# Kernel optimization log

Hardware: AMD Instinct MI355X
Metric: run time of the kernel (lower is better)

The kernel has to match this reference:

```python
import jax, jax.numpy as jnp
import numpy as np

ITERS = 5          # iter_node_counts
N, M, Z, E = 68, 46, 384, 368   # base VNs, base CNs, lifting size, total base edges
LLR_CLIP = 20.0    # allowed_llr_range.abs
BIG = 1e9


def setup_inputs() -> dict:
    key = jax.random.key(0)
    k1, k2, k3 = jax.random.split(key, 3)
    B = 64
    # channel LLRs, realistic AWGN-ish magnitudes
    xa = jax.random.normal(k1, (B, N, Z), dtype=jnp.float32) * 4.0
    edge_vn = jax.random.randint(k2, (E,), 0, N, dtype=jnp.int32)
    # regular check degree 8 so every check has >=2 edges (valid min-sum extrinsics)
    edge_cn = (jnp.arange(E, dtype=jnp.int32) % M)
    edge_shift = jax.random.randint(k3, (E,), 0, Z, dtype=jnp.int32)  # circulant shifts
    cn_weight = jnp.ones((ITERS,), dtype=jnp.float32)  # scalar CN weight per iteration
    return {"xa": xa, "cn_weight": cn_weight, "edge_vn": edge_vn,
            "edge_cn": edge_cn, "edge_shift": edge_shift}


def _qms5(x):
    # QMS q_bit=5 quantizer with straight-through estimator
    q = jnp.clip(jnp.round(x * 2.0) / 2.0, -7.5, 7.5)
    xc = jnp.clip(x, -7.5, 7.5)
    return xc + jax.lax.stop_gradient(q - xc)


def _decode(xa, cn_weight, edge_vn, edge_cn, edge_shift):
    B = xa.shape[0]
    xa_in = jnp.transpose(xa, (0, 2, 1))  # [B, Z, N]
    z = jnp.arange(Z)
    # lifting (Lift_Matrix1): cyclic shift each edge's Z copies; unlift is inverse
    idx_lift = ((z[:, None] - edge_shift[None, :]) % Z)[None]    # [1, Z, E]
    idx_unlift = ((z[:, None] + edge_shift[None, :]) % Z)[None]  # [1, Z, E]
    c2v = jnp.zeros((B, Z, E), dtype=xa.dtype)  # prev_llr (CN->VN messages)
    ch = jnp.moveaxis(xa_in, 2, 0)  # [N, B, Z]
    outs = []
    for it in range(ITERS):
        # --- odd layer (VN update): W_skipconn2even + W_odd2even ---
        vn_sum = jax.ops.segment_sum(jnp.moveaxis(c2v, 2, 0), edge_vn, num_segments=N)  # [N,B,Z]
        tot = ch + vn_sum                                  # total belief per VN
        v2c = jnp.moveaxis(tot[edge_vn], 0, 2) - c2v       # extrinsic, [B,Z,E]
        v2c = jnp.clip(v2c, -LLR_CLIP, LLR_CLIP)           # allowed_llr_range
        v2c = jnp.take_along_axis(v2c, idx_lift, axis=1)   # Lift_Matrix1
        # --- even layer (CN update, min-sum): W_even2odd ---
        vE = jnp.moveaxis(v2c, 2, 0)                       # [E, B, Z]
        mag = jnp.abs(vE)
        neg = (vE < 0).astype(jnp.int32)
        cnt = jax.ops.segment_sum(neg, edge_cn, num_segments=M)      # [M,B,Z]
        csign = (1 - 2 * (cnt % 2)).astype(vE.dtype)                 # sign product per CN
        min1 = jax.ops.segment_min(mag, edge_cn, num_segments=M)
        is_min = mag == min1[edge_cn]
        min2 = jax.ops.segment_min(jnp.where(is_min, BIG, mag), edge_cn, num_segments=M)
        ext_min = jnp.where(is_min, min2[edge_cn], min1[edge_cn])
        own_sign = jnp.where(vE < 0, -1.0, 1.0).astype(vE.dtype)
        ext = csign[edge_cn] * own_sign * ext_min          # extrinsic min-sum message
        ext = _qms5(cn_weight[it] * ext)                   # learned CN weight + QMS quantize
        c2v = jnp.moveaxis(ext, 0, 2)                      # [B,Z,E]
        c2v = jnp.take_along_axis(c2v, idx_unlift, axis=1) # Lift_Matrix2
        # --- output marginalization: W_output ---
        out = xa_in + jnp.moveaxis(
            jax.ops.segment_sum(jnp.moveaxis(c2v, 2, 0), edge_vn, num_segments=N), 0, 2)
        outs.append(out)
    return jnp.stack(outs)  # [ITERS, B, Z, N]


def reference(xa, cn_weight, edge_vn, edge_cn, edge_shift):
    return _decode(xa, cn_weight, edge_vn, edge_cn, edge_shift)
```

## Files before the change

### kernel.cpp

```cpp
#include <hip/hip_runtime.h>


#define ITERS 5
#define Nn 68
#define Mm 46
#define Zz 384
#define Ee 368
#define Bb 64
#define Kk 8
#define PADD 24
#define BIGF 1e9f

#define ROWB (Bb*Zz)
#define TOT_ELEMS (Nn*Bb*Zz)
#define C2V_BYTES ((Ee+1)*ROWB)
#define TOT_OFF   0
#define C2V_OFF   (TOT_ELEMS*4)
#define DEG_OFF   (C2V_OFF + C2V_BYTES)
#define VOFF_OFF  (DEG_OFF + 384)

#define R1 (TOT_ELEMS/4)
#define RC (C2V_BYTES/16)
#define NCOPY ((R1+RC)/256)

__global__ __launch_bounds__(256) void init_kernel(
    const float* __restrict__ xa, const int* __restrict__ edge_vn,
    float* __restrict__ tot, signed char* __restrict__ c2v,
    int* __restrict__ vn_deg, int* __restrict__ voff)
{
    int bid = blockIdx.x;
    if (bid < NCOPY) {
        int idx = bid * 256 + threadIdx.x;
        if (idx < R1) {
            int row = idx / 96;
            int zi  = idx - row * 96;
            int n = row >> 6;
            int b = row & 63;
            const float4* src = (const float4*)(xa + (size_t)(b * Nn + n) * Zz);
            ((float4*)tot)[idx] = src[zi];
        } else {
            int j = idx - R1;
            ((int4*)c2v)[j] = make_int4(0, 0, 0, 0);
        }
    } else {
        __shared__ int sev[Ee];
        for (int t = threadIdx.x; t < Ee; t += 256) sev[t] = edge_vn[t];
        __syncthreads();
        int n = threadIdx.x;
        if (n < Nn) {
            int d = 0;
            for (int e = 0; e < Ee; e++)
                if (sev[e] == n && d < PADD) voff[n * PADD + (d++)] = e * ROWB;
            vn_deg[n] = d;
            for (int j = d; j < PADD; j++) voff[n * PADD + j] = Ee * ROWB;
        }
    }
}

__global__ __launch_bounds__(384) void cn_kernel(
    const float* __restrict__ tot, signed char* __restrict__ c2v,
    const int* __restrict__ edge_vn, const int* __restrict__ edge_shift,
    const float* __restrict__ cn_weight, int it)
{
    const int cn = blockIdx.x;
    const int b  = blockIdx.y;
    const int zc = threadIdx.x;
    const float w = cn_weight[it];

    float v[Kk];
    int   off[Kk];
    float m1 = BIGF;
    unsigned sflip = 0u;

    #pragma unroll
    for (int k = 0; k < Kk; k++) {
        int e  = cn + k * Mm;
        int sh = edge_shift[e];
        int n  = edge_vn[e];
        int z  = zc - sh;
        z += (z >> 31) & Zz;
        int o = e * ROWB + b * Zz + z;
        off[k] = o;
        float t = tot[(n * Bb + b) * Zz + z];
        float c = 0.5f * (float)c2v[o];
        float x = t - c;
        x = fminf(20.0f, fmaxf(-20.0f, x));
        v[k] = x;
        if (x < 0.0f) sflip ^= 1u;
        m1 = fminf(m1, fabsf(x));
    }

    float m2 = BIGF;
    #pragma unroll
    for (int k = 0; k < Kk; k++) {
        float mag = fabsf(v[k]);
        if (mag != m1) m2 = fminf(m2, mag);
    }

    #pragma unroll
    for (int k = 0; k < Kk; k++) {
        float mag  = fabsf(v[k]);
        float emin = (mag == m1) ? m2 : m1;
        unsigned neg = sflip ^ ((v[k] < 0.0f) ? 1u : 0u);
        float ext = neg ? -emin : emin;
        float r = rintf(w * ext * 2.0f);
        r = fminf(15.0f, fmaxf(-15.0f, r));
        c2v[off[k]] = (signed char)(int)r;
    }
}

__global__ __launch_bounds__(256) void vn_kernel(
    const float* __restrict__ xa, const signed char* __restrict__ c2v,
    float* __restrict__ tot, float* __restrict__ out,
    const int* __restrict__ vn_deg, const int* __restrict__ voff,
    int write_tot)
{
    __shared__ float tile[17][65];
    const int b  = blockIdx.x;
    const int z0 = blockIdx.y * 64;
    const int n0 = blockIdx.z * 17;
    const int wave = threadIdx.x >> 6;
    const int lane = threadIdx.x & 63;
    const int z = z0 + lane;
    const int bz = b * Zz + z;

    for (int i = wave; i < 17; i += 4) {
        int n = __builtin_amdgcn_readfirstlane(n0 + i);
        int d = vn_deg[n];
        const int* vo = voff + n * PADD;
        int acc = 0;
        #pragma unroll
        for (int j = 0; j < 8; j++) acc += (int)c2v[vo[j] + bz];
        if (d > 8) {
            #pragma unroll
            for (int j = 8; j < 16; j++) acc += (int)c2v[vo[j] + bz];
        }
        if (d > 16) {
            #pragma unroll
            for (int j = 16; j < PADD; j++) acc += (int)c2v[vo[j] + bz];
        }
        float s = xa[(size_t)(b * Nn + n) * Zz + z] + 0.5f * (float)acc;
        if (write_tot) tot[(n * Bb + b) * Zz + z] = s;
        tile[i][lane] = s;
    }
    __syncthreads();

    float* dst = out + ((size_t)b * Zz + z0) * Nn + n0;
    for (int idx = threadIdx.x; idx < 17 * 64; idx += 256) {
        int zz = idx / 17;
        int nn = idx - zz * 17;
        dst[(size_t)zz * Nn + nn] = tile[nn][zz];
    }
}

extern "C" void kernel_launch(void* const* d_in, const int* in_sizes, int n_in,
                              void* d_out, int out_size, void* d_ws, size_t ws_size,
                              hipStream_t stream) {
    const float* xa        = (const float*)d_in[0];
    const float* cn_weight = (const float*)d_in[1];
    const int*   edge_vn   = (const int*)d_in[2];
    const int*   edge_shift= (const int*)d_in[4];
    float* out = (float*)d_out;

    char* ws = (char*)d_ws;
    float*       tot    = (float*)(ws + TOT_OFF);
    signed char* c2v    = (signed char*)(ws + C2V_OFF);
    int*         vn_deg = (int*)(ws + DEG_OFF);
    int*         voff   = (int*)(ws + VOFF_OFF);

    init_kernel<<<NCOPY + 1, 256, 0, stream>>>(xa, edge_vn, tot, c2v, vn_deg, voff);

    for (int it = 0; it < ITERS; it++) {
        cn_kernel<<<dim3(Mm, Bb), 384, 0, stream>>>(tot, c2v, edge_vn, edge_shift,
                                                    cn_weight, it);
        vn_kernel<<<dim3(Bb, Zz / 64, 4), 256, 0, stream>>>(
            xa, c2v, tot, out + (size_t)it * Bb * Zz * Nn,
            vn_deg, voff, (it != ITERS - 1) ? 1 : 0);
    }
}
```

Before: 194.7 us.

## Skip init copy and c2v zeroing via offset-biased bytes; vectorize VN loads

The full copy of xa into tot and the zeroing of the whole c2v buffer are removed. Iteration 0 of the CN kernel now reads xa directly and ignores c2v. c2v is stored as unsigned bytes with a +32 bias, so only the padding row needs initialising (to 32). The CN kernel handles two batch rows per block, and the VN kernel processes two z values per thread with 16-bit and float2 loads, changing its tiling to 128x9. This trades extra bias arithmetic and a tail check on the last n-block for less init traffic and fewer, wider memory accesses.

```diff
diff --git a/kernel.cpp b/kernel.cpp
--- a/kernel.cpp
+++ b/kernel.cpp
@@ -19,29 +19,14 @@
 #define DEG_OFF   (C2V_OFF + C2V_BYTES)
 #define VOFF_OFF  (DEG_OFF + 384)
 
-#define R1 (TOT_ELEMS/4)
-#define RC (C2V_BYTES/16)
-#define NCOPY ((R1+RC)/256)
-
 __global__ __launch_bounds__(256) void init_kernel(
-    const float* __restrict__ xa, const int* __restrict__ edge_vn,
-    float* __restrict__ tot, signed char* __restrict__ c2v,
+    const int* __restrict__ edge_vn, unsigned char* __restrict__ c2v,
     int* __restrict__ vn_deg, int* __restrict__ voff)
 {
-    int bid = blockIdx.x;
-    if (bid < NCOPY) {
-        int idx = bid * 256 + threadIdx.x;
-        if (idx < R1) {
-            int row = idx / 96;
-            int zi  = idx - row * 96;
-            int n = row >> 6;
-            int b = row & 63;
-            const float4* src = (const float4*)(xa + (size_t)(b * Nn + n) * Zz);
-            ((float4*)tot)[idx] = src[zi];
-        } else {
-            int j = idx - R1;
-            ((int4*)c2v)[j] = make_int4(0, 0, 0, 0);
-        }
+    if (blockIdx.x == 0) {
+        int4* p = (int4*)(c2v + (size_t)Ee * ROWB);
+        const int4 v = make_int4(0x20202020, 0x20202020, 0x20202020, 0x20202020);
+        for (int i = threadIdx.x; i < ROWB / 16; i += 256) p[i] = v;
     } else {
         __shared__ int sev[Ee];
         for (int t = threadIdx.x; t < Ee; t += 256) sev[t] = edge_vn[t];
@@ -58,19 +43,21 @@
 }
 
 __global__ __launch_bounds__(384) void cn_kernel(
-    const float* __restrict__ tot, signed char* __restrict__ c2v,
+    const float* __restrict__ belief,
+    unsigned char* __restrict__ c2v,
     const int* __restrict__ edge_vn, const int* __restrict__ edge_shift,
     const float* __restrict__ cn_weight, int it)
 {
     const int cn = blockIdx.x;
-    const int b  = blockIdx.y;
+    const int b0 = blockIdx.y * 2;
     const int zc = threadIdx.x;
     const float w = cn_weight[it];
+    const bool it0 = (it == 0);
 
-    float v[Kk];
-    int   off[Kk];
-    float m1 = BIGF;
-    unsigned sflip = 0u;
+    float v[2][Kk];
+    int   off[2][Kk];
+    float m1[2] = {BIGF, BIGF};
+    unsigned sf[2] = {0u, 0u};
 
     #pragma unroll
     for (int k = 0; k < Kk; k++) {
@@ -79,77 +66,103 @@
         int n  = edge_vn[e];
         int z  = zc - sh;
         z += (z >> 31) & Zz;
-        int o = e * ROWB + b * Zz + z;
-        off[k] = o;
-        float t = tot[(n * Bb + b) * Zz + z];
-        float c = 0.5f * (float)c2v[o];
-        float x = t - c;
-        x = fminf(20.0f, fmaxf(-20.0f, x));
-        v[k] = x;
-        if (x < 0.0f) sflip ^= 1u;
-        m1 = fminf(m1, fabsf(x));
-    }
-
-    float m2 = BIGF;
-    #pragma unroll
-    for (int k = 0; k < Kk; k++) {
-        float mag = fabsf(v[k]);
-        if (mag != m1) m2 = fminf(m2, mag);
+        #pragma unroll
+        for (int bb = 0; bb < 2; bb++) {
+            int b = b0 + bb;
+            int o = e * ROWB + b * Zz + z;
+            off[bb][k] = o;
+            float x;
+            if (it0) {
+                x = belief[(b * Nn + n) * Zz + z];
+            } else {
+                float t = belief[(n * Bb + b) * Zz + z];
+                x = t - 0.5f * (float)((int)c2v[o] - 32);
+            }
+            x = fminf(20.0f, fmaxf(-20.0f, x));
+            v[bb][k] = x;
+            sf[bb] ^= (x < 0.0f) ? 1u : 0u;
+            m1[bb] = fminf(m1[bb], fabsf(x));
+        }
     }
 
     #pragma unroll
-    for (int k = 0; k < Kk; k++) {
-        float mag  = fabsf(v[k]);
-        float emin = (mag == m1) ? m2 : m1;
-        unsigned neg = sflip ^ ((v[k] < 0.0f) ? 1u : 0u);
-        float ext = neg ? -emin : emin;
-        float r = rintf(w * ext * 2.0f);
-        r = fminf(15.0f, fmaxf(-15.0f, r));
-        c2v[off[k]] = (signed char)(int)r;
+    for (int bb = 0; bb < 2; bb++) {
+        float m2 = BIGF;
+        #pragma unroll
+        for (int k = 0; k < Kk; k++) {
+            float mag = fabsf(v[bb][k]);
+            if (mag != m1[bb]) m2 = fminf(m2, mag);
+        }
+        #pragma unroll
+        for (int k = 0; k < Kk; k++) {
+            float mag  = fabsf(v[bb][k]);
+            float emin = (mag == m1[bb]) ? m2 : m1[bb];
+            unsigned neg = sf[bb] ^ ((v[bb][k] < 0.0f) ? 1u : 0u);
+            float ext = neg ? -emin : emin;
+            float r = rintf(w * ext * 2.0f);
+            r = fminf(15.0f, fmaxf(-15.0f, r));
+            c2v[off[bb][k]] = (unsigned char)((int)r + 32);
+        }
     }
 }
 
 __global__ __launch_bounds__(256) void vn_kernel(
-    const float* __restrict__ xa, const signed char* __restrict__ c2v,
+    const float* __restrict__ xa, const unsigned char* __restrict__ c2v,
     float* __restrict__ tot, float* __restrict__ out,
     const int* __restrict__ vn_deg, const int* __restrict__ voff,
     int write_tot)
 {
-    __shared__ float tile[17][65];
+    __shared__ float tile[9][130];
     const int b  = blockIdx.x;
-    const int z0 = blockIdx.y * 64;
-    const int n0 = blockIdx.z * 17;
+    const int z0 = blockIdx.y * 128;
+    const int n0 = blockIdx.z * 9;
     const int wave = threadIdx.x >> 6;
     const int lane = threadIdx.x & 63;
-    const int z = z0 + lane;
+    const int z  = z0 + 2 * lane;
     const int bz = b * Zz + z;
 
-    for (int i = wave; i < 17; i += 4) {
+    for (int i = wave; i < 9; i += 4) {
+        if (n0 + i >= Nn) break;
         int n = __builtin_amdgcn_readfirstlane(n0 + i);
         int d = vn_deg[n];
         const int* vo = voff + n * PADD;
-        int acc = 0;
+        int aL = 0, aH = 0, L = 8;
         #pragma unroll
-        for (int j = 0; j < 8; j++) acc += (int)c2v[vo[j] + bz];
+        for (int j = 0; j < 8; j++) {
+            unsigned u = *(const unsigned short*)(c2v + (vo[j] + bz));
+            aL += u & 0xFFu; aH += u >> 8;
+        }
         if (d > 8) {
+            L = 16;
             #pragma unroll
-            for (int j = 8; j < 16; j++) acc += (int)c2v[vo[j] + bz];
+            for (int j = 8; j < 16; j++) {
+                unsigned u = *(const unsigned short*)(c2v + (vo[j] + bz));
+                aL += u & 0xFFu; aH += u >> 8;
+            }
+            if (d > 16) {
+                L = 24;
+                #pragma unroll
+                for (int j = 16; j < PADD; j++) {
+                    unsigned u = *(const unsigned short*)(c2v + (vo[j] + bz));
+                    aL += u & 0xFFu; aH += u >> 8;
+                }
+            }
         }
-        if (d > 16) {
-            #pragma unroll
-            for (int j = 16; j < PADD; j++) acc += (int)c2v[vo[j] + bz];
-        }
-        float s = xa[(size_t)(b * Nn + n) * Zz + z] + 0.5f * (float)acc;
-        if (write_tot) tot[(n * Bb + b) * Zz + z] = s;
-        tile[i][lane] = s;
+        float2 x = *(const float2*)(xa + ((size_t)b * Nn + n) * Zz + z);
+        float sL = x.x + 0.5f * (float)(aL - 32 * L);
+        float sH = x.y + 0.5f * (float)(aH - 32 * L);
+        if (write_tot)
+            *(float2*)(tot + (n * Bb + b) * Zz + z) = make_float2(sL, sH);
+        *(float2*)&tile[i][2 * lane] = make_float2(sL, sH);
     }
     __syncthreads();
 
     float* dst = out + ((size_t)b * Zz + z0) * Nn + n0;
-    for (int idx = threadIdx.x; idx < 17 * 64; idx += 256) {
-        int zz = idx / 17;
-        int nn = idx - zz * 17;
-        dst[(size_t)zz * Nn + nn] = tile[nn][zz];
+    const int nmax = (Nn - n0 < 9) ? (Nn - n0) : 9;
+    for (int idx = threadIdx.x; idx < 128 * 9; idx += 256) {
+        int zz = idx / 9;
+        int nn = idx - zz * 9;
+        if (nn < nmax) dst[(size_t)zz * Nn + nn] = tile[nn][zz];
     }
 }
 
@@ -163,17 +176,18 @@
     float* out = (float*)d_out;
 
     char* ws = (char*)d_ws;
-    float*       tot    = (float*)(ws + TOT_OFF);
-    signed char* c2v    = (signed char*)(ws + C2V_OFF);
-    int*         vn_deg = (int*)(ws + DEG_OFF);
-    int*         voff   = (int*)(ws + VOFF_OFF);
+    float*         tot    = (float*)(ws + TOT_OFF);
+    unsigned char* c2v    = (unsigned char*)(ws + C2V_OFF);
+    int*           vn_deg = (int*)(ws + DEG_OFF);
+    int*           voff   = (int*)(ws + VOFF_OFF);
 
-    init_kernel<<<NCOPY + 1, 256, 0, stream>>>(xa, edge_vn, tot, c2v, vn_deg, voff);
+    init_kernel<<<2, 256, 0, stream>>>(edge_vn, c2v, vn_deg, voff);
 
     for (int it = 0; it < ITERS; it++) {
-        cn_kernel<<<dim3(Mm, Bb), 384, 0, stream>>>(tot, c2v, edge_vn, edge_shift,
-                                                    cn_weight, it);
-        vn_kernel<<<dim3(Bb, Zz / 64, 4), 256, 0, stream>>>(
+        const float* belief = (it == 0) ? xa : tot;
+        cn_kernel<<<dim3(Mm, Bb / 2), 384, 0, stream>>>(belief, c2v, edge_vn,
+                                                        edge_shift, cn_weight, it);
+        vn_kernel<<<dim3(Bb, Zz / 128, 8), 256, 0, stream>>>(
             xa, c2v, tot, out + (size_t)it * Bb * Zz * Nn,
             vn_deg, voff, (it != ITERS - 1) ? 1 : 0);
     }
```

Measured after the change: 220.4 us. 13.2% more time.

## Fuse init, CN and VN updates into one persistent per-batch kernel

Applied to the files above, without the earlier changes.

Replaces the init kernel and the ten alternating CN/VN launches with one kernel. It runs one 1024-thread block per batch element and loops over all iterations internally, separated by block barriers. Edge tables and VN adjacency are built in shared memory with atomics. The first iteration reads xa directly, so the full c2v and tot initialisation copies are no longer needed. This removes launch overhead and global init traffic and keeps each batch's state in a cache-friendly slice, but it uses only 64 blocks on a GPU with many more CUs and adds many block barriers.

```diff
diff --git a/kernel.cpp b/kernel.cpp
--- a/kernel.cpp
+++ b/kernel.cpp
@@ -11,145 +11,127 @@
 #define PADD 24
 #define BIGF 1e9f
 
-#define ROWB (Bb*Zz)
-#define TOT_ELEMS (Nn*Bb*Zz)
-#define C2V_BYTES ((Ee+1)*ROWB)
-#define TOT_OFF   0
-#define C2V_OFF   (TOT_ELEMS*4)
-#define DEG_OFF   (C2V_OFF + C2V_BYTES)
-#define VOFF_OFF  (DEG_OFF + 384)
+#define SLICE   (Ee*Zz)
+#define SLICE_P (SLICE + Zz)
+#define NZ      (Nn*Zz)
+#define TOT_OFF 0
+#define C2V_OFF (Bb*NZ*4)
 
-#define R1 (TOT_ELEMS/4)
-#define RC (C2V_BYTES/16)
-#define NCOPY ((R1+RC)/256)
+__global__ __launch_bounds__(1024) void fused_kernel(
+    const float* __restrict__ xa,
+    const float* __restrict__ cn_weight,
+    const int* __restrict__ edge_vn, const int* __restrict__ edge_shift,
+    float* __restrict__ out,
+    float* __restrict__ tot_g, signed char* __restrict__ c2v_g)
+{
+    __shared__ int   s_ev[Ee];
+    __shared__ int   s_sh[Ee];
+    __shared__ int   s_deg[Nn];
+    __shared__ int   s_voff[Nn * PADD];
+    __shared__ float tile[17][Zz + 1];
 
-__global__ __launch_bounds__(256) void init_kernel(
-    const float* __restrict__ xa, const int* __restrict__ edge_vn,
-    float* __restrict__ tot, signed char* __restrict__ c2v,
-    int* __restrict__ vn_deg, int* __restrict__ voff)
-{
-    int bid = blockIdx.x;
-    if (bid < NCOPY) {
-        int idx = bid * 256 + threadIdx.x;
-        if (idx < R1) {
-            int row = idx / 96;
-            int zi  = idx - row * 96;
-            int n = row >> 6;
-            int b = row & 63;
-            const float4* src = (const float4*)(xa + (size_t)(b * Nn + n) * Zz);
-            ((float4*)tot)[idx] = src[zi];
-        } else {
-            int j = idx - R1;
-            ((int4*)c2v)[j] = make_int4(0, 0, 0, 0);
-        }
-    } else {
-        __shared__ int sev[Ee];
-        for (int t = threadIdx.x; t < Ee; t += 256) sev[t] = edge_vn[t];
-        __syncthreads();
-        int n = threadIdx.x;
-        if (n < Nn) {
-            int d = 0;
-            for (int e = 0; e < Ee; e++)
-                if (sev[e] == n && d < PADD) voff[n * PADD + (d++)] = e * ROWB;
-            vn_deg[n] = d;
-            for (int j = d; j < PADD; j++) voff[n * PADD + j] = Ee * ROWB;
-        }
+    const int b    = blockIdx.x;
+    const int tid  = threadIdx.x;
+    const int wave = tid >> 6;
+    const int lane = tid & 63;
+    const float* xa_b  = xa + (size_t)b * NZ;
+    float*       tot_b = tot_g + (size_t)b * NZ;
+    signed char* c2v_b = c2v_g + (size_t)b * SLICE_P;
+
+    if (tid < Ee) { s_ev[tid] = edge_vn[tid]; s_sh[tid] = edge_shift[tid]; }
+    else if (tid < Ee + Nn) s_deg[tid - Ee] = 0;
+    __syncthreads();
+    if (tid < Ee) {
+        int n = s_ev[tid];
+        int slot = atomicAdd(&s_deg[n], 1);
+        if (slot < PADD) s_voff[n * PADD + slot] = tid * Zz;
     }
-}
-
-__global__ __launch_bounds__(384) void cn_kernel(
-    const float* __restrict__ tot, signed char* __restrict__ c2v,
-    const int* __restrict__ edge_vn, const int* __restrict__ edge_shift,
-    const float* __restrict__ cn_weight, int it)
-{
-    const int cn = blockIdx.x;
-    const int b  = blockIdx.y;
-    const int zc = threadIdx.x;
-    const float w = cn_weight[it];
-
-    float v[Kk];
-    int   off[Kk];
-    float m1 = BIGF;
-    unsigned sflip = 0u;
-
-    #pragma unroll
-    for (int k = 0; k < Kk; k++) {
-        int e  = cn + k * Mm;
-        int sh = edge_shift[e];
-        int n  = edge_vn[e];
-        int z  = zc - sh;
-        z += (z >> 31) & Zz;
-        int o = e * ROWB + b * Zz + z;
-        off[k] = o;
-        float t = tot[(n * Bb + b) * Zz + z];
-        float c = 0.5f * (float)c2v[o];
-        float x = t - c;
-        x = fminf(20.0f, fmaxf(-20.0f, x));
-        v[k] = x;
-        if (x < 0.0f) sflip ^= 1u;
-        m1 = fminf(m1, fabsf(x));
-    }
-
-    float m2 = BIGF;
-    #pragma unroll
-    for (int k = 0; k < Kk; k++) {
-        float mag = fabsf(v[k]);
-        if (mag != m1) m2 = fminf(m2, mag);
-    }
-
-    #pragma unroll
-    for (int k = 0; k < Kk; k++) {
-        float mag  = fabsf(v[k]);
-        float emin = (mag == m1) ? m2 : m1;
-        unsigned neg = sflip ^ ((v[k] < 0.0f) ? 1u : 0u);
-        float ext = neg ? -emin : emin;
-        float r = rintf(w * ext * 2.0f);
-        r = fminf(15.0f, fmaxf(-15.0f, r));
-        c2v[off[k]] = (signed char)(int)r;
-    }
-}
-
-__global__ __launch_bounds__(256) void vn_kernel(
-    const float* __restrict__ xa, const signed char* __restrict__ c2v,
-    float* __restrict__ tot, float* __restrict__ out,
-    const int* __restrict__ vn_deg, const int* __restrict__ voff,
-    int write_tot)
-{
-    __shared__ float tile[17][65];
-    const int b  = blockIdx.x;
-    const int z0 = blockIdx.y * 64;
-    const int n0 = blockIdx.z * 17;
-    const int wave = threadIdx.x >> 6;
-    const int lane = threadIdx.x & 63;
-    const int z = z0 + lane;
-    const int bz = b * Zz + z;
-
-    for (int i = wave; i < 17; i += 4) {
-        int n = __builtin_amdgcn_readfirstlane(n0 + i);
-        int d = vn_deg[n];
-        const int* vo = voff + n * PADD;
-        int acc = 0;
-        #pragma unroll
-        for (int j = 0; j < 8; j++) acc += (int)c2v[vo[j] + bz];
-        if (d > 8) {
-            #pragma unroll
-            for (int j = 8; j < 16; j++) acc += (int)c2v[vo[j] + bz];
-        }
-        if (d > 16) {
-            #pragma unroll
-            for (int j = 16; j < PADD; j++) acc += (int)c2v[vo[j] + bz];
-        }
-        float s = xa[(size_t)(b * Nn + n) * Zz + z] + 0.5f * (float)acc;
-        if (write_tot) tot[(n * Bb + b) * Zz + z] = s;
-        tile[i][lane] = s;
+    if (tid >= 512 && tid < 512 + Zz / 4)
+        ((int*)(c2v_b + SLICE))[tid - 512] = 0;
+    __syncthreads();
+    if (tid < Nn) {
+        int d = s_deg[tid];
+        if (d > PADD) { d = PADD; s_deg[tid] = PADD; }
+        for (int j = d; j < PADD; j++) s_voff[tid * PADD + j] = SLICE;
     }
     __syncthreads();
 
-    float* dst = out + ((size_t)b * Zz + z0) * Nn + n0;
-    for (int idx = threadIdx.x; idx < 17 * 64; idx += 256) {
-        int zz = idx / 17;
-        int nn = idx - zz * 17;
-        dst[(size_t)zz * Nn + nn] = tile[nn][zz];
+    #pragma unroll 1
+    for (int it = 0; it < ITERS; it++) {
+        const float w = cn_weight[it];
+        const float* belief = it ? tot_b : xa_b;
+        const bool sub = (it != 0);
+
+        for (int t = wave; t < Mm * 6; t += 16) {
+            int cn = t / 6;
+            int zc = (t - cn * 6) * 64 + lane;
+            float v[Kk]; int off[Kk];
+            float m1 = BIGF; unsigned sflip = 0u;
+            #pragma unroll
+            for (int k = 0; k < Kk; k++) {
+                int e  = cn + k * Mm;
+                int sh = s_sh[e], n = s_ev[e];
+                int z  = zc - sh; z += (z >> 31) & Zz;
+                int o  = e * Zz + z;
+                off[k] = o;
+                float x = belief[n * Zz + z];
+                if (sub) x -= 0.5f * (float)c2v_b[o];
+                x = fminf(20.0f, fmaxf(-20.0f, x));
+                v[k] = x;
+                if (x < 0.0f) sflip ^= 1u;
+                m1 = fminf(m1, fabsf(x));
+            }
+            float m2 = BIGF;
+            #pragma unroll
+            for (int k = 0; k < Kk; k++) {
+                float mag = fabsf(v[k]);
+                if (mag != m1) m2 = fminf(m2, mag);
+            }
+            #pragma unroll
+            for (int k = 0; k < Kk; k++) {
+                float mag  = fabsf(v[k]);
+                float emin = (mag == m1) ? m2 : m1;
+                unsigned neg = sflip ^ ((v[k] < 0.0f) ? 1u : 0u);
+                float ext = neg ? -emin : emin;
+                float r = rintf(w * ext * 2.0f);
+                r = fminf(15.0f, fmaxf(-15.0f, r));
+                c2v_b[off[k]] = (signed char)(int)r;
+            }
+        }
+        __syncthreads();
+
+        float* outp = out + (size_t)it * (Bb * (size_t)NZ) + (size_t)b * NZ;
+        for (int g = 0; g < 4; g++) {
+            const int n0 = g * 17;
+            for (int t = wave; t < 17 * 6; t += 16) {
+                int i = t / 6;
+                int z = (t - i * 6) * 64 + lane;
+                int n = n0 + i;
+                int d = s_deg[n];
+                const int* vo = s_voff + n * PADD;
+                int acc = 0;
+                #pragma unroll
+                for (int j = 0; j < 8; j++) acc += (int)c2v_b[vo[j] + z];
+                if (d > 8) {
+                    #pragma unroll
+                    for (int j = 8; j < 16; j++) acc += (int)c2v_b[vo[j] + z];
+                }
+                if (d > 16) {
+                    #pragma unroll
+                    for (int j = 16; j < PADD; j++) acc += (int)c2v_b[vo[j] + z];
+                }
+                float s = xa_b[n * Zz + z] + 0.5f * (float)acc;
+                if (it < ITERS - 1) tot_b[n * Zz + z] = s;
+                tile[i][z] = s;
+            }
+            __syncthreads();
+            for (int idx = tid; idx < 17 * Zz; idx += 1024) {
+                int zz = idx / 17;
+                int nn = idx - zz * 17;
+                outp[zz * Nn + n0 + nn] = tile[nn][zz];
+            }
+            __syncthreads();
+        }
     }
 }
 
@@ -163,18 +145,9 @@
     float* out = (float*)d_out;
 
     char* ws = (char*)d_ws;
-    float*       tot    = (float*)(ws + TOT_OFF);
-    signed char* c2v    = (signed char*)(ws + C2V_OFF);
-    int*         vn_deg = (int*)(ws + DEG_OFF);
-    int*         voff   = (int*)(ws + VOFF_OFF);
+    float*       tot_g = (float*)(ws + TOT_OFF);
+    signed char* c2v_g = (signed char*)(ws + C2V_OFF);
 
-    init_kernel<<<NCOPY + 1, 256, 0, stream>>>(xa, edge_vn, tot, c2v, vn_deg, voff);
-
-    for (int it = 0; it < ITERS; it++) {
-        cn_kernel<<<dim3(Mm, Bb), 384, 0, stream>>>(tot, c2v, edge_vn, edge_shift,
-                                                    cn_weight, it);
-        vn_kernel<<<dim3(Bb, Zz / 64, 4), 256, 0, stream>>>(
-            xa, c2v, tot, out + (size_t)it * Bb * Zz * Nn,
-            vn_deg, voff, (it != ITERS - 1) ? 1 : 0);
-    }
+    fused_kernel<<<Bb, 1024, 0, stream>>>(xa, cn_weight, edge_vn, edge_shift,
+                                          out, tot_g, c2v_g);
 }
```

Measured after the change: 402.5 us. 2.07x slower.
